# Kernel optimization log

Hardware: AMD Instinct MI355X
Metric: run time of the kernel (lower is better)

Reference implementation:

```python
import jax, jax.numpy as jnp
import numpy as np

THETA = 10000.0


def apply_rope(x, token_position, theta=THETA):
    # x: [B, H, S, d_k] with interleaved even/odd pairs; token_position: [B, S]
    B, H, S, d_k = x.shape
    inv_freq = 1.0 / theta ** (jnp.arange(0, d_k, 2, dtype=jnp.float32) / d_k)  # [d_k/2]
    angles = token_position.astype(jnp.float32)[:, :, None] * inv_freq[None, None, :]  # [B,S,d_k/2]
    cos = jnp.cos(angles)[:, None, :, :]  # [B,1,S,d_k/2]
    sin = jnp.sin(angles)[:, None, :, :]
    xp = x.reshape(B, H, S, d_k // 2, 2)
    x_even, x_odd = xp[..., 0], xp[..., 1]
    rot_even = x_even * cos - x_odd * sin
    rot_odd = x_even * sin + x_odd * cos
    return jnp.stack([rot_even, rot_odd], axis=-1).reshape(B, H, S, d_k)


def setup_inputs() -> dict:
    key = jax.random.key(0)
    ks = jax.random.split(key, 6)
    B, S, D = 2, 2048, 2048
    x = jax.random.normal(ks[0], (B, S, D), dtype=jnp.float32)
    token_position = jnp.sort(jax.random.randint(ks[1], (B, S), 0, 2048), axis=-1).astype(jnp.int32)
    scale = 0.02
    WQ = jax.random.normal(ks[2], (D, D), dtype=jnp.float32) * scale
    WK = jax.random.normal(ks[3], (D, D), dtype=jnp.float32) * scale
    WV = jax.random.normal(ks[4], (D, D), dtype=jnp.float32) * scale
    WO = jax.random.normal(ks[5], (D, D), dtype=jnp.float32) * scale
    return {"x": x, "token_position": token_position, "WQ": WQ, "WK": WK, "WV": WV, "WO": WO}


def reference(x, token_position, WQ, WK, WV, WO):
    B, S, D = x.shape
    H = 16
    d_k = D // H

    def proj(W):
        return jnp.matmul(x, W).reshape(B, S, H, d_k).transpose(0, 2, 1, 3)  # [B,H,S,d_k]

    Q = apply_rope(proj(WQ), token_position)
    K = apply_rope(proj(WK), token_position)
    V = proj(WV)

    score = jnp.einsum('bhqd,bhkd->bhqk', Q, K) / jnp.sqrt(jnp.float32(d_k))
    causal = jnp.triu(jnp.full((S, S), -jnp.inf, dtype=jnp.float32), k=1)
    score = score + causal
    attn = jax.nn.softmax(score, axis=-1)  # stable max-sub softmax, same math
    out = jnp.einsum('bhqk,bhkd->bhqd', attn, V)
    out = out.transpose(0, 2, 1, 3).reshape(B, S, D)
    return jnp.matmul(out, WO)
```

## Files before the change

kernel.cpp:

```cpp
#include <hip/hip_runtime.h>
#include <hip/hip_bf16.h>
#include <cstdint>
#include <cstddef>

typedef unsigned short u16;
typedef __attribute__((ext_vector_type(4))) unsigned short u16x4;
typedef __attribute__((ext_vector_type(8))) unsigned short u16x8;
typedef __attribute__((ext_vector_type(8))) __bf16 bf16x8;
typedef __attribute__((ext_vector_type(4))) float f32x4;

#define MFMA16(a, b, c) __builtin_amdgcn_mfma_f32_16x16x32_bf16((a), (b), (c), 0, 0, 0)

__device__ __forceinline__ u16 f2bf(float f) {
  uint32_t u = __builtin_bit_cast(uint32_t, f);
  u += 0x7FFFu + ((u >> 16) & 1u);
  return (u16)(u >> 16);
}
__device__ __forceinline__ float bf2f(u16 h) {
  return __builtin_bit_cast(float, (uint32_t)h << 16);
}

typedef const __attribute__((address_space(1))) void gv_t;
typedef __attribute__((address_space(3))) void lv_t;
__device__ __forceinline__ void gload16(const void* g, void* l) {
  __builtin_amdgcn_global_load_lds((gv_t*)g, (lv_t*)l, 16, 0, 0);
}

__global__ void cvt_f32_to_bf16(const float* __restrict__ in, u16* __restrict__ out, int n4) {
  int i = blockIdx.x * 256 + threadIdx.x;
  if (i >= n4) return;
  float4 v = ((const float4*)in)[i];
  u16x4 o;
  o[0] = f2bf(v.x); o[1] = f2bf(v.y); o[2] = f2bf(v.z); o[3] = f2bf(v.w);
  ((u16x4*)out)[i] = o;
}

__global__ void transpose_cvt4(const float* __restrict__ w0, const float* __restrict__ w1,
                               const float* __restrict__ w2, const float* __restrict__ w3,
                               u16* __restrict__ outbase) {
  __shared__ float tile[32][33];
  const int z = blockIdx.z;
  const float* in = (z == 0) ? w0 : (z == 1) ? w1 : (z == 2) ? w2 : w3;
  u16* out = outbase + (size_t)z * 4194304;
  const int bx = blockIdx.x, by = blockIdx.y;
  const int tx = threadIdx.x, ty = threadIdx.y;
#pragma unroll
  for (int i = 0; i < 32; i += 8)
    tile[ty + i][tx] = in[(size_t)(by * 32 + ty + i) * 2048 + bx * 32 + tx];
  __syncthreads();
#pragma unroll
  for (int i = 0; i < 32; i += 8)
    out[(size_t)(bx * 32 + ty + i) * 2048 + by * 32 + tx] = f2bf(tile[tx][ty + i]);
}

__global__ void vtrans(const u16* __restrict__ in, u16* __restrict__ out) {
  __shared__ u16 tile[32][34];
  const int bx = blockIdx.x, by = blockIdx.y;
  const int tx = threadIdx.x, ty = threadIdx.y;
#pragma unroll
  for (int i = 0; i < 32; i += 8)
    tile[ty + i][tx] = in[(size_t)(by * 32 + ty + i) * 2048 + bx * 32 + tx];
  __syncthreads();
#pragma unroll
  for (int i = 0; i < 32; i += 8) {
    const int c = bx * 32 + ty + i;
    const int token = by * 32 + tx;
    out[(((size_t)(token >> 11) * 16 + (c >> 7)) * 128 + (c & 127)) * 2048 + (token & 2047)] =
        tile[tx][ty + i];
  }
}

template <int MODE>
__global__ __launch_bounds__(512, 1) void gemm8(const u16* __restrict__ A,
                                                const u16* __restrict__ Bt,
                                                void* __restrict__ Cv,
                                                const int* __restrict__ pos, int nbn) {
  constexpr int K = 2048;
  __shared__ __align__(16) u16 lds[73728];
  const int tid = threadIdx.x, lane = tid & 63;
  const int lo16 = lane & 15, hi = lane >> 4;
  const int wid = tid >> 6;
  const int wr = wid >> 1, wc = wid & 1;

  const int xcd = (int)blockIdx.x & 7;
  const int idx = (int)blockIdx.x >> 3;
  const int cpx = nbn >> 3;
  const int bn = (xcd * cpx + idx % cpx) * 128;
  const int bm = (idx / cpx) * 256;

  const int srow = tid >> 3;
  const int scol = ((tid & 7) ^ (srow & 7)) * 8;
  const u16* Arow = A + (size_t)(bm + srow) * K + scol;
  const u16* Brow = Bt + (size_t)(bn + srow) * K + scol;
  char* dstbase = (char*)lds + tid * 16;

#define STG_A(qb_, t_, r_) \
  gload16(Arow + (size_t)(r_) * 64 * K + (t_) * 64, dstbase + (qb_) * 49152 + (r_) * 8192)
#define STG_B(qb_, t_, r_) \
  gload16(Brow + (size_t)(r_) * 64 * K + (t_) * 64, dstbase + (qb_) * 49152 + 32768 + (r_) * 8192)

  f32x4 acc[4][4];
  const f32x4 z4 = {0.f, 0.f, 0.f, 0.f};
#pragma unroll
  for (int m = 0; m < 4; ++m)
#pragma unroll
    for (int n = 0; n < 4; ++n) acc[m][n] = z4;

  const int xork = lo16 & 7;
  const int aRow = (wr * 64 + lo16) * 128;
  const int bRow = 32768 + (wc * 64 + lo16) * 128;
  const int x0 = ((hi ^ xork)) << 4;
  const int x1 = (((4 + hi) ^ xork)) << 4;

  STG_A(0, 0, 0); STG_A(0, 0, 1); STG_A(0, 0, 2); STG_A(0, 0, 3);
  STG_B(0, 0, 0); STG_B(0, 0, 1);
  STG_A(1, 1, 0); STG_A(1, 1, 1); STG_A(1, 1, 2); STG_A(1, 1, 3);
  STG_B(1, 1, 0); STG_B(1, 1, 1);

  int q = 0;
  for (int t = 0; t < 32; ++t) {
    if (t < 31) {
      asm volatile("s_waitcnt vmcnt(6)" ::: "memory");
    } else {
      asm volatile("s_waitcnt vmcnt(0)" ::: "memory");
    }
    __builtin_amdgcn_s_barrier();
    __builtin_amdgcn_sched_barrier(0);
    const char* Aq = (const char*)lds + q * 49152;
    const int q2 = (q == 0) ? 2 : q - 1;

    bf16x8 a0[4], b0[4], a1[4], b1[4];
#pragma unroll
    for (int m = 0; m < 4; ++m) a0[m] = *(const bf16x8*)(Aq + aRow + m * 2048 + x0);
#pragma unroll
    for (int n = 0; n < 4; ++n) b0[n] = *(const bf16x8*)(Aq + bRow + n * 2048 + x0);
#pragma unroll
    for (int m = 0; m < 4; ++m) a1[m] = *(const bf16x8*)(Aq + aRow + m * 2048 + x1);
#pragma unroll
    for (int n = 0; n < 4; ++n) b1[n] = *(const bf16x8*)(Aq + bRow + n * 2048 + x1);

    if (t < 30) {
      STG_A(q2, t + 2, 0); STG_A(q2, t + 2, 1); STG_A(q2, t + 2, 2); STG_A(q2, t + 2, 3);
      STG_B(q2, t + 2, 0); STG_B(q2, t + 2, 1);
    }

    __builtin_amdgcn_s_setprio(1);
#pragma unroll
    for (int m = 0; m < 4; ++m)
#pragma unroll
      for (int n = 0; n < 4; ++n) acc[m][n] = MFMA16(a0[m], b0[n], acc[m][n]);
#pragma unroll
    for (int m = 0; m < 4; ++m)
#pragma unroll
      for (int n = 0; n < 4; ++n) acc[m][n] = MFMA16(a1[m], b1[n], acc[m][n]);
    __builtin_amdgcn_s_setprio(0);
    q = (q == 2) ? 0 : q + 1;
  }
#undef STG_A
#undef STG_B

  if constexpr (MODE == 2) {
    const int sect = bn >> 11;
    u16* Cq = (u16*)Cv + (size_t)sect * 8388608;
    const int cb = (bn & 2047) + wc * 64;
    if (sect < 2) {
      const float qsc = (sect == 0) ? 0.08838834764831845f : 1.0f;
      float freq[4];
#pragma unroll
      for (int n = 0; n < 4; ++n) {
        const int c = cb + n * 16 + lo16;
        freq[n] = exp2f((float)((c & 127) >> 1) * -0.2076205059304601f);
      }
      const float sg = (lo16 & 1) ? 1.f : -1.f;
#pragma unroll
      for (int m = 0; m < 4; ++m) {
        const int row = bm + wr * 64 + m * 16 + hi * 4;
#pragma unroll
        for (int r = 0; r < 4; ++r) {
          const float p = (float)pos[row + r];
#pragma unroll
          for (int n = 0; n < 4; ++n) {
            const float ang = p * freq[n];
            const float sn = __sinf(ang);
            const float cs = __cosf(ang);
            const float v = acc[m][n][r];
            const float pv = __shfl_xor(v, 1);
            Cq[(size_t)(row + r) * 2048 + cb + n * 16 + lo16] =
                f2bf((v * cs + sg * pv * sn) * qsc);
          }
        }
      }
    } else {
#pragma unroll
      for (int m = 0; m < 4; ++m)
#pragma unroll
        for (int n = 0; n < 4; ++n)
#pragma unroll
          for (int r = 0; r < 4; ++r)
            Cq[(size_t)(bm + wr * 64 + m * 16 + hi * 4 + r) * 2048 + cb + n * 16 + lo16] =
                f2bf(acc[m][n][r]);
    }
  } else {
    float* C = (float*)Cv;
    const int cb = bn + wc * 64;
#pragma unroll
    for (int m = 0; m < 4; ++m)
#pragma unroll
      for (int n = 0; n < 4; ++n)
#pragma unroll
        for (int r = 0; r < 4; ++r)
          C[(size_t)(bm + wr * 64 + m * 16 + hi * 4 + r) * 2048 + cb + n * 16 + lo16] =
              acc[m][n][r];
  }
}

__global__ __launch_bounds__(256, 2) void flash_attn4(const u16* __restrict__ Qb,
                                                      const u16* __restrict__ Kb,
                                                      const u16* __restrict__ VT,
                                                      u16* __restrict__ Ob) {
  constexpr int S = 2048, HD = 2048;
  const int g = (int)blockIdx.x;
  const int xcd = g & 7, slot = g >> 3;
  const int bh = xcd * 4 + (slot & 3);
  const int pairid = slot >> 2;
  const int b = bh >> 4, h = bh & 15;
  const int tid = threadIdx.x, lane = tid & 63, wid = tid >> 6;

  __shared__ u16 Ks[2][64 * 128];
  __shared__ u16 Vs[2][128 * 64];
  __shared__ u16 Ps[4][16 * 64];

  const size_t base = (size_t)b * S * HD + (size_t)h * 128;
  const u16* Qp = Qb + base;
  const u16* Kp = Kb + base;
  const u16* VTp = VT + (size_t)bh * 128 * S;
  u16* Op = Ob + base;

  const f32x4 z4 = {0.f, 0.f, 0.f, 0.f};
  const int kKv = (lane >> 4);
  const int kC16 = (lane & 15);
  const int vD = (lane >> 3);
  const int vC16 = (lane & 7);

#define STAGE(pb, kv0_)                                                                   \
  {                                                                                       \
    _Pragma("unroll") for (int c = 0; c < 4; ++c) {                                       \
      const int ch = wid * 4 + c;                                                         \
      {                                                                                   \
        const int kv = ch * 4 + kKv;                                                      \
        const int c16 = kC16 ^ (kv & 7);                                                  \
        gload16(Kp + (size_t)((kv0_) + kv) * HD + c16 * 8, (char*)Ks[pb] + ch * 1024);    \
      }                                                                                   \
      {                                                                                   \
        const int d = ch * 8 + vD;                                                        \
        const int c16 = vC16 ^ (d & 7);                                                   \
        gload16(VTp + (size_t)d * S + (kv0_) + c16 * 8, (char*)Vs[pb] + ch * 1024);       \
      }                                                                                   \
    }                                                                                     \
  }

#pragma unroll
  for (int half = 0; half < 2; ++half) {
    const int qt = half ? pairid : 31 - pairid;
    const int q0 = qt * 64;

    bf16x8 qf[4];
    {
      const int qr = q0 + wid * 16 + (lane & 15);
      const int kc = (lane >> 4) * 8;
#pragma unroll
      for (int kb = 0; kb < 4; ++kb)
        qf[kb] = *(const bf16x8*)(Qp + (size_t)qr * HD + kb * 32 + kc);
    }

    f32x4 accO[8];
#pragma unroll
    for (int d = 0; d < 8; ++d) accO[d] = z4;
    float m_r[4] = {-INFINITY, -INFINITY, -INFINITY, -INFINITY};
    float l_r[4] = {0.f, 0.f, 0.f, 0.f};

    STAGE(0, 0);
    __syncthreads();

    for (int t = 0; t <= qt; ++t) {
      const int cur = t & 1;
      const int kv0 = t * 64;
      if (t < qt) STAGE(cur ^ 1, kv0 + 64);

      const u16* Ksc = Ks[cur];
      const u16* Vsc = Vs[cur];
      f32x4 accS[4];
#pragma unroll
      for (int nb = 0; nb < 4; ++nb) accS[nb] = z4;

      __builtin_amdgcn_s_setprio(1);
#pragma unroll
      for (int nb = 0; nb < 4; ++nb) {
        const int kv = nb * 16 + (lane & 15);
#pragma unroll
        for (int kb = 0; kb < 4; ++kb) {
          const int c16 = (kb * 4 + (lane >> 4)) ^ (kv & 7);
          bf16x8 kf = *(const bf16x8*)((char*)Ksc + kv * 256 + c16 * 16);
          accS[nb] = MFMA16(qf[kb], kf, accS[nb]);
        }
      }
      __builtin_amdgcn_s_setprio(0);

      if (t == qt) {
#pragma unroll
        for (int nb = 0; nb < 4; ++nb) {
          const int kv = kv0 + nb * 16 + (lane & 15);
          const int qrow = q0 + wid * 16 + (lane >> 4) * 4;
#pragma unroll
          for (int j = 0; j < 4; ++j)
            if (kv > qrow + j) accS[nb][j] = -INFINITY;
        }
      }

      float lm[4];
#pragma unroll
      for (int j = 0; j < 4; ++j)
        lm[j] = fmaxf(fmaxf(accS[0][j], accS[1][j]), fmaxf(accS[2][j], accS[3][j]));
      const bool ok = (lm[0] <= m_r[0] + 8.f) && (lm[1] <= m_r[1] + 8.f) &&
                      (lm[2] <= m_r[2] + 8.f) && (lm[3] <= m_r[3] + 8.f);
      if (!__all(ok)) {
#pragma unroll
        for (int j = 0; j < 4; ++j) {
          float mx = lm[j];
#pragma unroll
          for (int off = 1; off < 16; off <<= 1) mx = fmaxf(mx, __shfl_xor(mx, off));
          const float mn = fmaxf(m_r[j], mx);
          const float sc = __expf(m_r[j] - mn);
          m_r[j] = mn;
          l_r[j] *= sc;
#pragma unroll
          for (int db = 0; db < 8; ++db) accO[db][j] *= sc;
        }
      }

      u16* Pw = &Ps[wid][0];
#pragma unroll
      for (int j = 0; j < 4; ++j) {
        float s = 0.f;
#pragma unroll
        for (int nb = 0; nb < 4; ++nb) {
          const float p = __expf(accS[nb][j] - m_r[j]);
          accS[nb][j] = p;
          s += p;
        }
        l_r[j] += s;
        const int ql = (lane >> 4) * 4 + j;
#pragma unroll
        for (int nb = 0; nb < 4; ++nb) {
          const int col = nb * 16 + (lane & 15);
          const int byteoff = ql * 128 + ((((col >> 3) ^ (ql & 7))) << 4) + (col & 7) * 2;
          *(u16*)((char*)Pw + byteoff) = f2bf(accS[nb][j]);
        }
      }

#pragma unroll
      for (int kb2 = 0; kb2 < 2; ++kb2) {
        const int ql = lane & 15;
        const int c16a = (kb2 * 4 + (lane >> 4)) ^ (ql & 7);
        bf16x8 pa = *(const bf16x8*)((char*)Pw + ql * 128 + c16a * 16);
        __builtin_amdgcn_s_setprio(1);
#pragma unroll
        for (int db = 0; db < 8; ++db) {
          const int d = db * 16 + (lane & 15);
          const int c16 = (kb2 * 4 + (lane >> 4)) ^ (d & 7);
          bf16x8 vf = *(const bf16x8*)((char*)Vsc + d * 128 + c16 * 16);
          accO[db] = MFMA16(pa, vf, accO[db]);
        }
        __builtin_amdgcn_s_setprio(0);
      }
      __syncthreads();
    }

    float inv[4];
#pragma unroll
    for (int j = 0; j < 4; ++j) {
      float l = l_r[j];
#pragma unroll
      for (int off = 1; off < 16; off <<= 1) l += __shfl_xor(l, off);
      inv[j] = 1.f / l;
    }
#pragma unroll
    for (int db = 0; db < 8; ++db)
#pragma unroll
      for (int j = 0; j < 4; ++j) {
        const int row = q0 + wid * 16 + (lane >> 4) * 4 + j;
        Op[(size_t)row * HD + db * 16 + (lane & 15)] = f2bf(accO[db][j] * inv[j]);
      }
  }
#undef STAGE
}

extern "C" void kernel_launch(void* const* d_in, const int* in_sizes, int n_in,
                              void* d_out, int out_size, void* d_ws, size_t ws_size,
                              hipStream_t stream) {
  const float* x  = (const float*)d_in[0];
  const int*   tp = (const int*)d_in[1];
  const float* WQ = (const float*)d_in[2];
  const float* WK = (const float*)d_in[3];
  const float* WV = (const float*)d_in[4];
  const float* WO = (const float*)d_in[5];

  const size_t MB = 1024 * 1024;
  if (ws_size < 112 * MB) return;
  char* ws = (char*)d_ws;
  u16* xb  = (u16*)(ws + 0 * MB);
  u16* wqt = (u16*)(ws + 16 * MB);
  u16* wot = (u16*)(ws + 40 * MB);
  u16* Qb  = (u16*)(ws + 48 * MB);
  u16* Kb  = (u16*)(ws + 64 * MB);
  u16* Vb  = (u16*)(ws + 80 * MB);
  u16* Obf = (u16*)(ws + 96 * MB);
  u16* VTb = xb;

  cvt_f32_to_bf16<<<8192, 256, 0, stream>>>(x, xb, 2097152);
  {
    dim3 g(64, 64, 4), blk(32, 8);
    transpose_cvt4<<<g, blk, 0, stream>>>(WQ, WK, WV, WO, wqt);
  }
  gemm8<2><<<768, 512, 0, stream>>>(xb, wqt, (void*)Qb, tp, 48);

  {
    dim3 g(64, 128), blk(32, 8);
    vtrans<<<g, blk, 0, stream>>>(Vb, VTb);
  }
  flash_attn4<<<512, 256, 0, stream>>>(Qb, Kb, VTb, Obf);

  gemm8<1><<<256, 512, 0, stream>>>(Obf, wot, d_out, nullptr, 16);
}
```

Measured before the change: 243.1 us.

## Fuse V transpose into QKV GEMM epilogue and relax attention barriers

The V projection epilogue now stages its output tile through LDS transposed and writes V directly in [b,h,d,token] layout. This removes the separate vtrans kernel and its extra round trip through global memory. The attention loop also swaps __syncthreads for explicit vmcnt waits plus s_barrier, so the next K/V prefetch can stay in flight while the current tile computes. The hand-set vmcnt counts depend on how many loads STAGE issues, so a wrong count would introduce a race.

```diff
diff --git a/kernel.cpp b/kernel.cpp
--- a/kernel.cpp
+++ b/kernel.cpp
@@ -51,23 +51,6 @@
 #pragma unroll
   for (int i = 0; i < 32; i += 8)
     out[(size_t)(bx * 32 + ty + i) * 2048 + by * 32 + tx] = f2bf(tile[tx][ty + i]);
-}
-
-__global__ void vtrans(const u16* __restrict__ in, u16* __restrict__ out) {
-  __shared__ u16 tile[32][34];
-  const int bx = blockIdx.x, by = blockIdx.y;
-  const int tx = threadIdx.x, ty = threadIdx.y;
-#pragma unroll
-  for (int i = 0; i < 32; i += 8)
-    tile[ty + i][tx] = in[(size_t)(by * 32 + ty + i) * 2048 + bx * 32 + tx];
-  __syncthreads();
-#pragma unroll
-  for (int i = 0; i < 32; i += 8) {
-    const int c = bx * 32 + ty + i;
-    const int token = by * 32 + tx;
-    out[(((size_t)(token >> 11) * 16 + (c >> 7)) * 128 + (c & 127)) * 2048 + (token & 2047)] =
-        tile[tx][ty + i];
-  }
 }
 
 template <int MODE>
@@ -191,14 +174,31 @@
         }
       }
     } else {
-#pragma unroll
-      for (int m = 0; m < 4; ++m)
-#pragma unroll
-        for (int n = 0; n < 4; ++n)
+      __syncthreads();
+#pragma unroll
+      for (int m = 0; m < 4; ++m) {
+#pragma unroll
+        for (int n = 0; n < 4; ++n) {
+          const int d = wc * 64 + n * 16 + lo16;
+          const int tokb = wr * 64 + m * 16 + hi * 4;
 #pragma unroll
           for (int r = 0; r < 4; ++r)
-            Cq[(size_t)(bm + wr * 64 + m * 16 + hi * 4 + r) * 2048 + cb + n * 16 + lo16] =
-                f2bf(acc[m][n][r]);
+            lds[d * 260 + tokb + r] = f2bf(acc[m][n][r]);
+        }
+      }
+      __syncthreads();
+      const int b = bm >> 11, hh = (bn & 2047) >> 7;
+      u16* vt = Cq + ((size_t)((b * 16 + hh) * 128)) * 2048 + (bm & 2047);
+#pragma unroll
+      for (int j = 0; j < 4; ++j) {
+        const int d = (tid >> 4) + j * 32;
+        const int t0 = (tid & 15) * 16;
+        const u16* src = lds + d * 260 + t0;
+        u16* dst = vt + (size_t)d * 2048 + t0;
+#pragma unroll
+        for (int w = 0; w < 4; ++w)
+          *(u16x4*)(dst + w * 4) = *(const u16x4*)(src + w * 4);
+      }
     }
   } else {
     float* C = (float*)Cv;
@@ -280,12 +280,18 @@
     float l_r[4] = {0.f, 0.f, 0.f, 0.f};
 
     STAGE(0, 0);
-    __syncthreads();
 
     for (int t = 0; t <= qt; ++t) {
       const int cur = t & 1;
       const int kv0 = t * 64;
-      if (t < qt) STAGE(cur ^ 1, kv0 + 64);
+      if (t < qt) {
+        STAGE(cur ^ 1, kv0 + 64);
+        asm volatile("s_waitcnt vmcnt(8)" ::: "memory");
+      } else {
+        asm volatile("s_waitcnt vmcnt(0)" ::: "memory");
+      }
+      __builtin_amdgcn_s_barrier();
+      __builtin_amdgcn_sched_barrier(0);
 
       const u16* Ksc = Ks[cur];
       const u16* Vsc = Vs[cur];
@@ -373,7 +379,8 @@
         }
         __builtin_amdgcn_s_setprio(0);
       }
-      __syncthreads();
+      __builtin_amdgcn_sched_barrier(0);
+      __builtin_amdgcn_s_barrier();
     }
 
     float inv[4];
@@ -413,9 +420,8 @@
   u16* wot = (u16*)(ws + 40 * MB);
   u16* Qb  = (u16*)(ws + 48 * MB);
   u16* Kb  = (u16*)(ws + 64 * MB);
-  u16* Vb  = (u16*)(ws + 80 * MB);
+  u16* VTb = (u16*)(ws + 80 * MB);
   u16* Obf = (u16*)(ws + 96 * MB);
-  u16* VTb = xb;
 
   cvt_f32_to_bf16<<<8192, 256, 0, stream>>>(x, xb, 2097152);
   {
@@ -424,10 +430,6 @@
   }
   gemm8<2><<<768, 512, 0, stream>>>(xb, wqt, (void*)Qb, tp, 48);
 
-  {
-    dim3 g(64, 128), blk(32, 8);
-    vtrans<<<g, blk, 0, stream>>>(Vb, VTb);
-  }
   flash_attn4<<<512, 256, 0, stream>>>(Qb, Kb, VTb, Obf);
 
   gemm8<1><<<256, 512, 0, stream>>>(Obf, wot, d_out, nullptr, 16);
```

After: 238.1 us. 1.02x faster.
